# Performance work log

Measured on AMD Instinct MI355X. Metric: run time of the kernel, lower is better.

## Reference

```python
import jax, jax.numpy as jnp
import numpy as np
import math

H = 8  # num_heads
# mock_theta_f Taylor coefficients: K(q) = 1 + q - 2q^2 + 3q^3
COEFFS = (1.0, 1.0, -2.0, 3.0)


def setup_inputs() -> dict:
    key = jax.random.key(0)
    ks = jax.random.split(key, 12)
    B, L, E = 2, 2048, 512
    s = 0.02
    return {
        "query": jax.random.normal(ks[0], (B, L, E), jnp.float32),
        "key_": jax.random.normal(ks[1], (B, L, E), jnp.float32),
        "value": jax.random.normal(ks[2], (B, L, E), jnp.float32),
        "Wq": jax.random.normal(ks[3], (E, E), jnp.float32) * s,
        "bq": jnp.zeros((E,), jnp.float32),
        "Wk": jax.random.normal(ks[4], (E, E), jnp.float32) * s,
        "bk": jnp.zeros((E,), jnp.float32),
        "Wv": jax.random.normal(ks[5], (E, E), jnp.float32) * s,
        "bv": jnp.zeros((E,), jnp.float32),
        "Wo": jax.random.normal(ks[6], (E, E), jnp.float32) * s,
        "bo": jnp.zeros((E,), jnp.float32),
        "log_tau": jnp.zeros((), jnp.float32),  # tau = exp(0) = 1.0
    }


def _horner(q):
    a0, a1, a2, a3 = COEFFS
    val = jnp.full_like(q, a3)
    val = q * val + a2
    val = q * val + a1
    val = q * val + a0
    return jnp.maximum(val, 0.0)


def _attn(query, key_, value, Wq, bq, Wk, bk, Wv, bv, Wo, bo, log_tau):
    B, L, E = query.shape
    S = key_.shape[1]
    Hd = E // H
    scale = math.sqrt(Hd)

    Q = (query @ Wq.T + bq).reshape(B, L, H, Hd).transpose(0, 2, 1, 3)  # (B,H,L,Hd)
    K = (key_ @ Wk.T + bk).reshape(B, S, H, Hd).transpose(0, 2, 1, 3)
    V = (value @ Wv.T + bv).reshape(B, S, H, Hd).transpose(0, 2, 1, 3)

    scores = jnp.einsum("bhld,bhsd->bhls", Q, K) / scale  # (B,H,L,S)

    tau = jnp.exp(log_tau)
    q = jax.nn.sigmoid(scores / tau)
    kv = _horner(q)

    # causal mask (is_causal=True): mask strict upper triangle
    causal = jnp.triu(jnp.ones((L, S), dtype=bool), k=1)  # (L,S)
    kv = jnp.where(causal[None, None], 0.0, kv)

    denom = jnp.sum(kv, axis=-1, keepdims=True)
    weights = kv / jnp.maximum(denom, 1e-12)

    out = jnp.einsum("bhls,bhsd->bhld", weights, V)  # (B,H,L,Hd)
    out = out.transpose(0, 2, 1, 3).reshape(B, L, E)
    return out @ Wo.T + bo


def reference(query, key_, value, Wq, bq, Wk, bk, Wv, bv, Wo, bo, log_tau):
    return _attn(query, key_, value, Wq, bq, Wk, bk, Wv, bv, Wo, bo, log_tau)
```

## Files before the change

kernel.cpp:

```cpp
#include <hip/hip_runtime.h>
#include <hip/hip_bf16.h>


typedef __attribute__((ext_vector_type(8))) __bf16 bf16x8;
typedef __attribute__((ext_vector_type(4))) __bf16 bf16x4;
typedef __attribute__((ext_vector_type(4))) float f32x4;

#define NB 2
#define NL 2048
#define NE 512
#define NH 8
#define HD 64
#define NROW (NB * NL)

__device__ __forceinline__ void gload16(const void* g, void* l) {
  __builtin_amdgcn_global_load_lds(
      (const __attribute__((address_space(1))) void*)g,
      (__attribute__((address_space(3))) void*)l, 16, 0, 0);
}

__global__ __launch_bounds__(256) void cvt_qkv(
    const float* __restrict__ q, const float* __restrict__ k,
    const float* __restrict__ v, __bf16* __restrict__ qo,
    __bf16* __restrict__ ko, __bf16* __restrict__ vo) {
  const int gid = blockIdx.x * 256 + threadIdx.x;
  const int seg = gid >> 19;
  const int i = gid & ((1 << 19) - 1);
  const float* s = seg == 0 ? q : (seg == 1 ? k : v);
  __bf16* d = seg == 0 ? qo : (seg == 1 ? ko : vo);
  float4 x = ((const float4*)s)[i];
  bf16x4 o = {(__bf16)x.x, (__bf16)x.y, (__bf16)x.z, (__bf16)x.w};
  ((bf16x4*)d)[i] = o;
}

__global__ __launch_bounds__(256) void cvt_w(
    const float* __restrict__ w0, const float* __restrict__ w1,
    const float* __restrict__ w2, const float* __restrict__ w3,
    __bf16* __restrict__ o0, __bf16* __restrict__ o1,
    __bf16* __restrict__ o2, __bf16* __restrict__ o3) {
  const int gid = blockIdx.x * 256 + threadIdx.x;
  const int seg = gid >> 16;
  const int i = gid & 0xFFFF;
  const float* s = seg == 0 ? w0 : (seg == 1 ? w1 : (seg == 2 ? w2 : w3));
  __bf16* d = seg == 0 ? o0 : (seg == 1 ? o1 : (seg == 2 ? o2 : o3));
  float4 x = ((const float4*)s)[i];
  bf16x4 o = {(__bf16)x.x, (__bf16)x.y, (__bf16)x.z, (__bf16)x.w};
  ((bf16x4*)d)[i] = o;
}

template <int MODE>
__device__ __forceinline__ void gemm_body(const __bf16* __restrict__ A,
                                          const __bf16* __restrict__ W,
                                          const float* __restrict__ bias,
                                          __bf16* __restrict__ outb,
                                          float* __restrict__ outf) {
  __shared__ __align__(16) __bf16 As[128 * 32];
  __shared__ __align__(16) __bf16 Ws[128 * 32];

  const int tid = threadIdx.x;
  const int lane = tid & 63, w = tid >> 6;
  const int lr = lane & 15, lg = lane >> 4;
  const int brow = blockIdx.y * 128, bcol = blockIdx.x * 128;
  const int wr = (w >> 1) * 64, wc = (w & 1) * 64;

  f32x4 zero4 = {0.f, 0.f, 0.f, 0.f};
  f32x4 acc[4][4];
#pragma unroll
  for (int i = 0; i < 4; ++i)
#pragma unroll
    for (int j = 0; j < 4; ++j) acc[i][j] = zero4;

  const int c0 = tid, c1 = tid + 256;
  const int r0 = c0 >> 2, cc0 = c0 & 3;
  const int r1 = c1 >> 2, cc1 = c1 & 3;

  for (int k0 = 0; k0 < NE; k0 += 32) {
    __syncthreads();
    gload16(A + (size_t)(brow + r0) * NE + k0 + cc0 * 8, As + c0 * 8);
    gload16(W + (size_t)(bcol + r0) * NE + k0 + cc0 * 8, Ws + c0 * 8);
    gload16(A + (size_t)(brow + r1) * NE + k0 + cc1 * 8, As + c1 * 8);
    gload16(W + (size_t)(bcol + r1) * NE + k0 + cc1 * 8, Ws + c1 * 8);
    __syncthreads();

    bf16x8 af[4], wf[4];
#pragma unroll
    for (int mi = 0; mi < 4; ++mi)
      af[mi] = *(const bf16x8*)(As + (wr + mi * 16 + lr) * 32 + lg * 8);
#pragma unroll
    for (int ni = 0; ni < 4; ++ni)
      wf[ni] = *(const bf16x8*)(Ws + (wc + ni * 16 + lr) * 32 + lg * 8);
#pragma unroll
    for (int mi = 0; mi < 4; ++mi)
#pragma unroll
      for (int ni = 0; ni < 4; ++ni)
        acc[mi][ni] = __builtin_amdgcn_mfma_f32_16x16x32_bf16(
            af[mi], wf[ni], acc[mi][ni], 0, 0, 0);
  }

#pragma unroll
  for (int mi = 0; mi < 4; ++mi) {
#pragma unroll
    for (int ni = 0; ni < 4; ++ni) {
      const int col = bcol + wc + ni * 16 + lr;
      const float bv = bias[col];
#pragma unroll
      for (int r = 0; r < 4; ++r) {
        const int row = brow + wr + mi * 16 + lg * 4 + r;
        const float v = acc[mi][ni][r] + bv;
        if (MODE == 0) {
          const int b = row >> 11, l = row & (NL - 1);
          const int h = col >> 6, d = col & 63;
          outb[(((size_t)b * NH + h) * NL + l) * HD + d] = (__bf16)v;
        } else if (MODE == 2) {
          const int b = row >> 11, l = row & (NL - 1);
          const int h = col >> 6, d = col & 63;
          outb[(((size_t)b * NH + h) * HD + d) * NL + l] = (__bf16)v;
        } else {
          outf[(size_t)row * NE + col] = v;
        }
      }
    }
  }
}

__global__ __launch_bounds__(256) void qkv_gemm(
    const __bf16* __restrict__ A0, const __bf16* __restrict__ A1,
    const __bf16* __restrict__ A2, const __bf16* __restrict__ W0,
    const __bf16* __restrict__ W1, const __bf16* __restrict__ W2,
    const float* __restrict__ b0, const float* __restrict__ b1,
    const float* __restrict__ b2, __bf16* __restrict__ O0,
    __bf16* __restrict__ O1, __bf16* __restrict__ O2) {
  const int z = blockIdx.z;
  if (z == 2) {
    gemm_body<2>(A2, W2, b2, O2, nullptr);
  } else {
    const __bf16* A = z == 0 ? A0 : A1;
    const __bf16* W = z == 0 ? W0 : W1;
    const float* bias = z == 0 ? b0 : b1;
    __bf16* O = z == 0 ? O0 : O1;
    gemm_body<0>(A, W, bias, O, nullptr);
  }
}

__global__ __launch_bounds__(256) void out_gemm(const __bf16* __restrict__ A,
                                                const __bf16* __restrict__ W,
                                                const float* __restrict__ bias,
                                                float* __restrict__ outf) {
  gemm_body<1>(A, W, bias, nullptr, outf);
}

__global__ __launch_bounds__(256) void attn_kernel(
    const __bf16* __restrict__ Qg, const __bf16* __restrict__ Kg,
    const __bf16* __restrict__ VTg, float* __restrict__ numg,
    float* __restrict__ deng, const float* __restrict__ log_tau) {
  __shared__ __align__(16) __bf16 Kt[64][72];
  __shared__ __align__(16) __bf16 Vt[64][72];
  __shared__ __align__(16) __bf16 Pl[4][16][72];

  const int j = blockIdx.x;
  int qb, c;
  if (j < 32) {
    c = 0; qb = j;
  } else if (j < 60) {
    c = 1; qb = j - 28;
  } else if (j < 84) {
    c = 2; qb = j - 52;
  } else if (j < 104) {
    c = 3; qb = j - 72;
  } else if (j < 120) {
    c = 4; qb = j - 88;
  } else if (j < 132) {
    c = 5; qb = j - 100;
  } else if (j < 140) {
    c = 6; qb = j - 108;
  } else {
    c = 7; qb = j - 112;
  }
  const int bh = blockIdx.y;
  const __bf16* Qh = Qg + (size_t)bh * NL * HD;
  const __bf16* Kh = Kg + (size_t)bh * NL * HD;
  const __bf16* Vth = VTg + (size_t)bh * HD * NL;

  const int tid = threadIdx.x;
  const int lane = tid & 63, w = tid >> 6;
  const int lr = lane & 15, lg = lane >> 4;
  const float ninv = -1.44269504f / (8.0f * __expf(log_tau[0]));

  const int q0 = qb * 64;
  const int qrow = q0 + w * 16 + lr;
  bf16x8 qf[2];
  qf[0] = *(const bf16x8*)(Qh + (size_t)qrow * HD + lg * 8);
  qf[1] = *(const bf16x8*)(Qh + (size_t)qrow * HD + 32 + lg * 8);

  f32x4 zero4 = {0.f, 0.f, 0.f, 0.f};
  f32x4 o_acc[4];
#pragma unroll
  for (int n = 0; n < 4; ++n) o_acc[n] = zero4;
  float den[4] = {0.f, 0.f, 0.f, 0.f};

  const int t0 = c * 4;
  const int t1 = min(t0 + 4, qb + 1);

  const int kr0 = tid >> 3, kc0 = (tid & 7) * 8;

  bf16x8 kpa = *(const bf16x8*)(Kh + (size_t)(t0 * 64 + kr0) * HD + kc0);
  bf16x8 kpb = *(const bf16x8*)(Kh + (size_t)(t0 * 64 + kr0 + 32) * HD + kc0);
  bf16x8 vpa = *(const bf16x8*)(Vth + (size_t)kr0 * NL + t0 * 64 + kc0);
  bf16x8 vpb = *(const bf16x8*)(Vth + (size_t)(kr0 + 32) * NL + t0 * 64 + kc0);

  for (int t = t0; t < t1; ++t) {
    const int kv0 = t * 64;
    __syncthreads();
    *(bf16x8*)&Kt[kr0][kc0] = kpa;
    *(bf16x8*)&Kt[kr0 + 32][kc0] = kpb;
    *(bf16x8*)&Vt[kr0][kc0] = vpa;
    *(bf16x8*)&Vt[kr0 + 32][kc0] = vpb;
    __syncthreads();

    if (t + 1 < t1) {
      const int kn = (t + 1) * 64;
      kpa = *(const bf16x8*)(Kh + (size_t)(kn + kr0) * HD + kc0);
      kpb = *(const bf16x8*)(Kh + (size_t)(kn + kr0 + 32) * HD + kc0);
      vpa = *(const bf16x8*)(Vth + (size_t)kr0 * NL + kn + kc0);
      vpb = *(const bf16x8*)(Vth + (size_t)(kr0 + 32) * NL + kn + kc0);
    }

    f32x4 sacc[4];
#pragma unroll
    for (int si = 0; si < 4; ++si) sacc[si] = zero4;
#pragma unroll
    for (int kk = 0; kk < 2; ++kk) {
#pragma unroll
      for (int si = 0; si < 4; ++si) {
        bf16x8 kf = *(const bf16x8*)&Kt[si * 16 + lr][kk * 32 + lg * 8];
        sacc[si] = __builtin_amdgcn_mfma_f32_16x16x32_bf16(qf[kk], kf,
                                                           sacc[si], 0, 0, 0);
      }
    }

#pragma unroll
    for (int si = 0; si < 4; ++si) {
      const int sg = kv0 + si * 16 + lr;
#pragma unroll
      for (int r = 0; r < 4; ++r) {
        const int qg = q0 + w * 16 + lg * 4 + r;
        const float e = __builtin_amdgcn_exp2f(sacc[si][r] * ninv);
        const float qs = __builtin_amdgcn_rcpf(1.0f + e);
        float kvv = fmaf(qs, fmaf(qs, fmaf(qs, 3.0f, -2.0f), 1.0f), 1.0f);
        kvv = fmaxf(kvv, 0.0f);
        if (sg > qg) kvv = 0.0f;
        const __bf16 kb = (__bf16)kvv;
        Pl[w][lg * 4 + r][si * 16 + lr] = kb;
        sacc[si][r] = (float)kb;
      }
    }

#pragma unroll
    for (int r = 0; r < 4; ++r) {
      float rsv = sacc[0][r] + sacc[1][r] + sacc[2][r] + sacc[3][r];
#pragma unroll
      for (int m = 1; m < 16; m <<= 1) rsv += __shfl_xor(rsv, m, 64);
      den[r] += rsv;
    }

#pragma unroll
    for (int kk = 0; kk < 2; ++kk) {
      bf16x8 pf = *(const bf16x8*)&Pl[w][lr][kk * 32 + lg * 8];
#pragma unroll
      for (int n = 0; n < 4; ++n) {
        bf16x8 vf = *(const bf16x8*)&Vt[n * 16 + lr][kk * 32 + lg * 8];
        o_acc[n] = __builtin_amdgcn_mfma_f32_16x16x32_bf16(pf, vf, o_acc[n],
                                                           0, 0, 0);
      }
    }
  }

  const int orow = q0 + w * 16 + lg * 4;
  if (lr == 0) {
#pragma unroll
    for (int r = 0; r < 4; ++r)
      atomicAdd(&deng[(size_t)bh * NL + orow + r], den[r]);
  }
#pragma unroll
  for (int n = 0; n < 4; ++n) {
    const int col = n * 16 + lr;
#pragma unroll
    for (int r = 0; r < 4; ++r)
      atomicAdd(&numg[((size_t)bh * NL + orow + r) * HD + col], o_acc[n][r]);
  }
}

__global__ __launch_bounds__(256) void combine_kernel(
    const float* __restrict__ numg, const float* __restrict__ deng,
    __bf16* __restrict__ AO) {
  const int gid = blockIdx.x * 256 + threadIdx.x;
  const int d4 = gid & 15;
  const int row = gid >> 4;
  const int bh = row >> 11, l = row & (NL - 1);
  const int b = bh >> 3, h = bh & 7;
  f32x4 n4 = ((const f32x4*)numg)[gid];
  const float idv = __builtin_amdgcn_rcpf(fmaxf(deng[row], 1e-12f));
  bf16x4 o = {(__bf16)(n4[0] * idv), (__bf16)(n4[1] * idv),
              (__bf16)(n4[2] * idv), (__bf16)(n4[3] * idv)};
  *(bf16x4*)&AO[((size_t)b * NL + l) * NE + h * HD + d4 * 4] = o;
}

extern "C" void kernel_launch(void* const* d_in, const int* in_sizes, int n_in,
                              void* d_out, int out_size, void* d_ws,
                              size_t ws_size, hipStream_t stream) {
  const float* query = (const float*)d_in[0];
  const float* key_ = (const float*)d_in[1];
  const float* value = (const float*)d_in[2];
  const float* Wq = (const float*)d_in[3];
  const float* bq = (const float*)d_in[4];
  const float* Wk = (const float*)d_in[5];
  const float* bk = (const float*)d_in[6];
  const float* Wv = (const float*)d_in[7];
  const float* bv = (const float*)d_in[8];
  const float* Wo = (const float*)d_in[9];
  const float* bo = (const float*)d_in[10];
  const float* log_tau = (const float*)d_in[11];

  char* ws = (char*)d_ws;
  const size_t MB = 1024 * 1024;
  __bf16* xb = (__bf16*)(ws + 0 * MB);
  __bf16* kxb = (__bf16*)(ws + 4 * MB);
  __bf16* vxb = (__bf16*)(ws + 8 * MB);
  __bf16* wqb = (__bf16*)(ws + 12 * MB);
  __bf16* wkb = (__bf16*)(ws + 12 * MB + 512 * 1024);
  __bf16* wvb = (__bf16*)(ws + 13 * MB);
  __bf16* wob = (__bf16*)(ws + 13 * MB + 512 * 1024);
  __bf16* Qh = (__bf16*)(ws + 14 * MB);
  __bf16* Kh = (__bf16*)(ws + 18 * MB);
  __bf16* VT = (__bf16*)(ws + 22 * MB);
  __bf16* AO = (__bf16*)(ws + 26 * MB);
  float* numb = (float*)(ws + 0 * MB);
  float* denb = (float*)(ws + 8 * MB);

  cvt_qkv<<<3 * (1 << 19) / 256, 256, 0, stream>>>(query, key_, value, xb, kxb,
                                                   vxb);
  cvt_w<<<4 * (1 << 16) / 256, 256, 0, stream>>>(Wq, Wk, Wv, Wo, wqb, wkb, wvb,
                                                 wob);

  dim3 gq(NE / 128, NROW / 128, 3);
  qkv_gemm<<<gq, 256, 0, stream>>>(xb, kxb, vxb, wqb, wkb, wvb, bq, bk, bv, Qh,
                                   Kh, VT);

  hipMemsetAsync(ws, 0, 8 * MB + 128 * 1024, stream);

  dim3 ga(144, NB * NH);
  attn_kernel<<<ga, 256, 0, stream>>>(Qh, Kh, VT, numb, denb, log_tau);

  combine_kernel<<<2048, 256, 0, stream>>>(numb, denb, AO);

  dim3 gg(NE / 128, NROW / 128);
  out_gemm<<<gg, 256, 0, stream>>>(AO, wob, bo, (float*)d_out);
}
```

Baseline: 93.05 us.

## Use 128-row query tiles with 512-thread blocks sharing K/V loads

The attention kernel now processes 128 query rows per block with 8 waves instead of 64 rows with 4 waves. Each K/V tile staged into shared memory is therefore reused by twice as many query rows, and each thread loads half as much. Waves whose rows lie entirely before a KV tile skip its compute via an early continue. Block scheduling becomes a reversed loop-based mapping over 72 blocks, which halves the grid and may lower occupancy and load balance.

```diff
diff --git a/kernel.cpp b/kernel.cpp
--- a/kernel.cpp
+++ b/kernel.cpp
@@ -149,32 +149,20 @@
   gemm_body<1>(A, W, bias, nullptr, outf);
 }
 
-__global__ __launch_bounds__(256) void attn_kernel(
+__global__ __launch_bounds__(512) void attn_kernel(
     const __bf16* __restrict__ Qg, const __bf16* __restrict__ Kg,
     const __bf16* __restrict__ VTg, float* __restrict__ numg,
     float* __restrict__ deng, const float* __restrict__ log_tau) {
   __shared__ __align__(16) __bf16 Kt[64][72];
   __shared__ __align__(16) __bf16 Vt[64][72];
-  __shared__ __align__(16) __bf16 Pl[4][16][72];
-
-  const int j = blockIdx.x;
-  int qb, c;
-  if (j < 32) {
-    c = 0; qb = j;
-  } else if (j < 60) {
-    c = 1; qb = j - 28;
-  } else if (j < 84) {
-    c = 2; qb = j - 52;
-  } else if (j < 104) {
-    c = 3; qb = j - 72;
-  } else if (j < 120) {
-    c = 4; qb = j - 88;
-  } else if (j < 132) {
-    c = 5; qb = j - 100;
-  } else if (j < 140) {
-    c = 6; qb = j - 108;
-  } else {
-    c = 7; qb = j - 112;
+  __shared__ __align__(16) __bf16 Pl[8][16][72];
+
+  int jj = 71 - blockIdx.x;
+  int qi = 0, c = 0;
+  for (int k = 0; k < 16; ++k) {
+    const int n = (k >> 1) + 1;
+    if (jj < n) { qi = k; c = jj; break; }
+    jj -= n;
   }
   const int bh = blockIdx.y;
   const __bf16* Qh = Qg + (size_t)bh * NL * HD;
@@ -186,7 +174,7 @@
   const int lr = lane & 15, lg = lane >> 4;
   const float ninv = -1.44269504f / (8.0f * __expf(log_tau[0]));
 
-  const int q0 = qb * 64;
+  const int q0 = qi * 128;
   const int qrow = q0 + w * 16 + lr;
   bf16x8 qf[2];
   qf[0] = *(const bf16x8*)(Qh + (size_t)qrow * HD + lg * 8);
@@ -199,31 +187,28 @@
   float den[4] = {0.f, 0.f, 0.f, 0.f};
 
   const int t0 = c * 4;
-  const int t1 = min(t0 + 4, qb + 1);
+  const int t1 = min(t0 + 4, 2 * qi + 2);
+  const int wq_hi = q0 + w * 16 + 15;
 
   const int kr0 = tid >> 3, kc0 = (tid & 7) * 8;
 
   bf16x8 kpa = *(const bf16x8*)(Kh + (size_t)(t0 * 64 + kr0) * HD + kc0);
-  bf16x8 kpb = *(const bf16x8*)(Kh + (size_t)(t0 * 64 + kr0 + 32) * HD + kc0);
   bf16x8 vpa = *(const bf16x8*)(Vth + (size_t)kr0 * NL + t0 * 64 + kc0);
-  bf16x8 vpb = *(const bf16x8*)(Vth + (size_t)(kr0 + 32) * NL + t0 * 64 + kc0);
 
   for (int t = t0; t < t1; ++t) {
     const int kv0 = t * 64;
     __syncthreads();
     *(bf16x8*)&Kt[kr0][kc0] = kpa;
-    *(bf16x8*)&Kt[kr0 + 32][kc0] = kpb;
     *(bf16x8*)&Vt[kr0][kc0] = vpa;
-    *(bf16x8*)&Vt[kr0 + 32][kc0] = vpb;
     __syncthreads();
 
     if (t + 1 < t1) {
       const int kn = (t + 1) * 64;
       kpa = *(const bf16x8*)(Kh + (size_t)(kn + kr0) * HD + kc0);
-      kpb = *(const bf16x8*)(Kh + (size_t)(kn + kr0 + 32) * HD + kc0);
       vpa = *(const bf16x8*)(Vth + (size_t)kr0 * NL + kn + kc0);
-      vpb = *(const bf16x8*)(Vth + (size_t)(kr0 + 32) * NL + kn + kc0);
-    }
+    }
+
+    if (kv0 > wq_hi) continue;
 
     f32x4 sacc[4];
 #pragma unroll
@@ -348,8 +333,8 @@
 
   hipMemsetAsync(ws, 0, 8 * MB + 128 * 1024, stream);
 
-  dim3 ga(144, NB * NH);
-  attn_kernel<<<ga, 256, 0, stream>>>(Qh, Kh, VT, numb, denb, log_tau);
+  dim3 ga(72, NB * NH);
+  attn_kernel<<<ga, 512, 0, stream>>>(Qh, Kh, VT, numb, denb, log_tau);
 
   combine_kernel<<<2048, 256, 0, stream>>>(numb, denb, AO);
 
```

After: 97.22 us. 1.04x slower.

## Replace atomic split-K accumulation with per-job slots and a reducing combine

Applied to the files above, without the earlier changes.

The attention kernel now writes each block's partial numerator and denominator to a private workspace slot instead of issuing float atomicAdds into a shared buffer. The combine kernel sums the slots belonging to each query block before normalising. This removes the memset and atomic contention, at the cost of a larger workspace and more read traffic in combine. The path is selected only when the workspace is at least 55 MB, otherwise the old atomic path runs.

```diff
diff --git a/kernel.cpp b/kernel.cpp
--- a/kernel.cpp
+++ b/kernel.cpp
@@ -12,6 +12,7 @@
 #define NH 8
 #define HD 64
 #define NROW (NB * NL)
+#define NJOB 144
 
 __device__ __forceinline__ void gload16(const void* g, void* l) {
   __builtin_amdgcn_global_load_lds(
@@ -149,6 +150,7 @@
   gemm_body<1>(A, W, bias, nullptr, outf);
 }
 
+template <int SLOTTED>
 __global__ __launch_bounds__(256) void attn_kernel(
     const __bf16* __restrict__ Qg, const __bf16* __restrict__ Kg,
     const __bf16* __restrict__ VTg, float* __restrict__ numg,
@@ -275,19 +277,60 @@
     }
   }
 
-  const int orow = q0 + w * 16 + lg * 4;
-  if (lr == 0) {
-#pragma unroll
-    for (int r = 0; r < 4; ++r)
-      atomicAdd(&deng[(size_t)bh * NL + orow + r], den[r]);
-  }
-#pragma unroll
-  for (int n = 0; n < 4; ++n) {
-    const int col = n * 16 + lr;
-#pragma unroll
-    for (int r = 0; r < 4; ++r)
-      atomicAdd(&numg[((size_t)bh * NL + orow + r) * HD + col], o_acc[n][r]);
-  }
+  if (SLOTTED) {
+    float* nslot = numg + (((size_t)bh * NJOB + j) << 12);
+    const int lrow = w * 16 + lg * 4;
+    if (lr == 0) {
+      float* dslot = deng + (((size_t)bh * NJOB + j) << 6);
+#pragma unroll
+      for (int r = 0; r < 4; ++r) dslot[lrow + r] = den[r];
+    }
+#pragma unroll
+    for (int n = 0; n < 4; ++n) {
+      const int col = n * 16 + lr;
+#pragma unroll
+      for (int r = 0; r < 4; ++r) nslot[(lrow + r) * 64 + col] = o_acc[n][r];
+    }
+  } else {
+    const int orow = q0 + w * 16 + lg * 4;
+    if (lr == 0) {
+#pragma unroll
+      for (int r = 0; r < 4; ++r)
+        atomicAdd(&deng[(size_t)bh * NL + orow + r], den[r]);
+    }
+#pragma unroll
+    for (int n = 0; n < 4; ++n) {
+      const int col = n * 16 + lr;
+#pragma unroll
+      for (int r = 0; r < 4; ++r)
+        atomicAdd(&numg[((size_t)bh * NL + orow + r) * HD + col], o_acc[n][r]);
+    }
+  }
+}
+
+__global__ __launch_bounds__(256) void combine_slotted(
+    const float* __restrict__ numS, const float* __restrict__ denS,
+    __bf16* __restrict__ AO) {
+  const int gid = blockIdx.x * 256 + threadIdx.x;
+  const int d4 = gid & 15;
+  const int row = gid >> 4;
+  const int bh = row >> 11, l = row & (NL - 1);
+  const int b = bh >> 3, h = bh & 7;
+  const int qb = l >> 6, lrow = l & 63;
+  const int nc = (qb >> 2) + 1;
+
+  f32x4 acc = {0.f, 0.f, 0.f, 0.f};
+  float d = 0.f;
+  for (int c = 0; c < nc; ++c) {
+    const int jj = qb + 2 * c * (15 - c);
+    const size_t sb = (size_t)bh * NJOB + jj;
+    acc += *(const f32x4*)(numS + ((sb << 6) + lrow) * 64 + d4 * 4);
+    d += denS[(sb << 6) + lrow];
+  }
+  const float idv = __builtin_amdgcn_rcpf(fmaxf(d, 1e-12f));
+  bf16x4 o = {(__bf16)(acc[0] * idv), (__bf16)(acc[1] * idv),
+              (__bf16)(acc[2] * idv), (__bf16)(acc[3] * idv)};
+  *(bf16x4*)&AO[((size_t)b * NL + l) * NE + h * HD + d4 * 4] = o;
 }
 
 __global__ __launch_bounds__(256) void combine_kernel(
@@ -323,19 +366,37 @@
 
   char* ws = (char*)d_ws;
   const size_t MB = 1024 * 1024;
+  const bool slotted = (ws_size >= 55 * MB);
+
   __bf16* xb = (__bf16*)(ws + 0 * MB);
   __bf16* kxb = (__bf16*)(ws + 4 * MB);
   __bf16* vxb = (__bf16*)(ws + 8 * MB);
-  __bf16* wqb = (__bf16*)(ws + 12 * MB);
-  __bf16* wkb = (__bf16*)(ws + 12 * MB + 512 * 1024);
-  __bf16* wvb = (__bf16*)(ws + 13 * MB);
-  __bf16* wob = (__bf16*)(ws + 13 * MB + 512 * 1024);
-  __bf16* Qh = (__bf16*)(ws + 14 * MB);
-  __bf16* Kh = (__bf16*)(ws + 18 * MB);
-  __bf16* VT = (__bf16*)(ws + 22 * MB);
-  __bf16* AO = (__bf16*)(ws + 26 * MB);
-  float* numb = (float*)(ws + 0 * MB);
-  float* denb = (float*)(ws + 8 * MB);
+
+  __bf16 *wqb, *wkb, *wvb, *wob, *Qh, *Kh, *VT, *AO;
+  float *numb, *denb;
+  if (slotted) {
+    numb = (float*)(ws + 0 * MB);
+    denb = (float*)(ws + 36 * MB);
+    wqb = (__bf16*)(ws + 37 * MB);
+    wkb = (__bf16*)(ws + 37 * MB + 512 * 1024);
+    wvb = (__bf16*)(ws + 38 * MB);
+    wob = (__bf16*)(ws + 38 * MB + 512 * 1024);
+    Qh = (__bf16*)(ws + 39 * MB);
+    Kh = (__bf16*)(ws + 43 * MB);
+    VT = (__bf16*)(ws + 47 * MB);
+    AO = (__bf16*)(ws + 51 * MB);
+  } else {
+    numb = (float*)(ws + 0 * MB);
+    denb = (float*)(ws + 8 * MB);
+    wqb = (__bf16*)(ws + 12 * MB);
+    wkb = (__bf16*)(ws + 12 * MB + 512 * 1024);
+    wvb = (__bf16*)(ws + 13 * MB);
+    wob = (__bf16*)(ws + 13 * MB + 512 * 1024);
+    Qh = (__bf16*)(ws + 14 * MB);
+    Kh = (__bf16*)(ws + 18 * MB);
+    VT = (__bf16*)(ws + 22 * MB);
+    AO = (__bf16*)(ws + 26 * MB);
+  }
 
   cvt_qkv<<<3 * (1 << 19) / 256, 256, 0, stream>>>(query, key_, value, xb, kxb,
                                                    vxb);
@@ -346,12 +407,15 @@
   qkv_gemm<<<gq, 256, 0, stream>>>(xb, kxb, vxb, wqb, wkb, wvb, bq, bk, bv, Qh,
                                    Kh, VT);
 
-  hipMemsetAsync(ws, 0, 8 * MB + 128 * 1024, stream);
-
-  dim3 ga(144, NB * NH);
-  attn_kernel<<<ga, 256, 0, stream>>>(Qh, Kh, VT, numb, denb, log_tau);
-
-  combine_kernel<<<2048, 256, 0, stream>>>(numb, denb, AO);
+  dim3 ga(NJOB, NB * NH);
+  if (slotted) {
+    attn_kernel<1><<<ga, 256, 0, stream>>>(Qh, Kh, VT, numb, denb, log_tau);
+    combine_slotted<<<2048, 256, 0, stream>>>(numb, denb, AO);
+  } else {
+    hipMemsetAsync(ws, 0, 8 * MB + 128 * 1024, stream);
+    attn_kernel<0><<<ga, 256, 0, stream>>>(Qh, Kh, VT, numb, denb, log_tau);
+    combine_kernel<<<2048, 256, 0, stream>>>(numb, denb, AO);
+  }
 
   dim3 gg(NE / 128, NROW / 128);
   out_gemm<<<gg, 256, 0, stream>>>(AO, wob, bo, (float*)d_out);
```

Result: faster. 82.24 us (-11.6%).
